# Kernel optimization log

Hardware: AMD Instinct MI355X
Metric: run time of the kernel (lower is better)

Reference implementation:

```python
import jax, jax.numpy as jnp
import numpy as np

HID = 32
R = 3
B = 2
IN = 64
N = 100000
E = 1600000
G = 256


def setup_inputs() -> dict:
    key = jax.random.key(0)
    ks = jax.random.split(key, 16)
    x = jax.random.normal(ks[0], (N, IN), dtype=jnp.float32)
    src = jax.random.randint(ks[1], (E,), 0, N)
    dst = jax.random.randint(ks[2], (E,), 0, N)
    etype = jax.random.randint(ks[3], (E,), 0, R)
    graph_ids = jnp.sort(jax.random.randint(ks[4], (N,), 0, G))
    s = 0.05
    basis1 = jax.random.normal(ks[5], (B, IN, HID), dtype=jnp.float32) * s   # layer 1 basis
    basis_r = jax.random.normal(ks[6], (3, B, HID, HID), dtype=jnp.float32) * s  # layers 2-4
    w_comp = jax.random.normal(ks[7], (4, R, B), dtype=jnp.float32) * s     # per-layer basis coeffs
    loop1 = jax.random.normal(ks[8], (IN, HID), dtype=jnp.float32) * s
    loop_r = jax.random.normal(ks[9], (3, HID, HID), dtype=jnp.float32) * s
    bias = jnp.zeros((4, HID), dtype=jnp.float32)
    lin1_w = jax.random.normal(ks[10], (4 * HID, 64), dtype=jnp.float32) * s
    lin1_b = jnp.zeros((64,), dtype=jnp.float32)
    lin2_w = jax.random.normal(ks[11], (64, 1), dtype=jnp.float32) * s
    lin2_b = jnp.zeros((1,), dtype=jnp.float32)
    return dict(x=x, basis1=basis1, basis_r=basis_r, w_comp=w_comp, loop1=loop1,
                loop_r=loop_r, bias=bias, lin1_w=lin1_w, lin1_b=lin1_b,
                lin2_w=lin2_w, lin2_b=lin2_b, src=src, dst=dst, etype=etype,
                graph_ids=graph_ids, num_graphs=G)


def _rel_conv(h, basis, comp, loop_w, b, src, dst, etype, n_nodes):
    # basis-decomposed relation weights: W[r] = sum_b comp[r,b] * basis[b]
    W = jnp.einsum('rb,bio->rio', comp, basis)            # [R, in, out]
    h_rel = jnp.einsum('ni,rio->rno', h, W)               # [R, N, out]
    msg = h_rel[etype, src]                               # [E, out] edge-typed gather
    agg = jax.ops.segment_sum(msg, dst, num_segments=n_nodes)
    return agg + h @ loop_w + b                           # self-loop + bias


def reference(x, basis1, basis_r, w_comp, loop1, loop_r, bias,
              lin1_w, lin1_b, lin2_w, lin2_b,
              src, dst, etype, graph_ids, num_graphs):
    n = x.shape[0]
    h = jnp.tanh(_rel_conv(x, basis1, w_comp[0], loop1, bias[0], src, dst, etype, n))
    states = [h]
    for i in range(3):
        h = jnp.tanh(_rel_conv(h, basis_r[i], w_comp[i + 1], loop_r[i], bias[i + 1],
                               src, dst, etype, n))
        states.append(h)
    feat = jnp.concatenate(states, axis=1)                # [N, 128]
    # mean-pool nodes per graph (diff_pooling ~ dgl mean_nodes)
    summed = jax.ops.segment_sum(feat, graph_ids, num_segments=num_graphs)
    counts = jax.ops.segment_sum(jnp.ones((n,), feat.dtype), graph_ids,
                                 num_segments=num_graphs)
    pooled = summed / jnp.maximum(counts, 1.0)[:, None]   # [G, 128]
    hdn = jax.nn.relu(pooled @ lin1_w + lin1_b)
    out = jax.nn.sigmoid(hdn @ lin2_w + lin2_b)
    return out[:, 0]
```

## Files before the change

### kernel.cpp

```cpp
#include <hip/hip_runtime.h>
#include <cstdint>
#include <cmath>

#define DLO_BITS 7
#define DLO_MASK 127

__global__ __launch_bounds__(256) void prep_w1(
    const float* __restrict__ basis1,
    const float* __restrict__ w_comp,
    float* __restrict__ W1)
{
    int tid = blockIdx.x * 256 + threadIdx.x;
    if (tid < 6144) {
        int r = tid / 2048, io = tid % 2048;
        W1[tid] = w_comp[r*2] * basis1[io] + w_comp[r*2+1] * basis1[2048 + io];
    }
}

__global__ __launch_bounds__(256) void count_kernel(
    const int* __restrict__ dst, int* __restrict__ bcnt, int E, int NB)
{
    __shared__ int cnt[1024];
    for (int i = threadIdx.x; i < NB; i += 256) cnt[i] = 0;
    __syncthreads();
    int base = blockIdx.x * 4096;
    #pragma unroll
    for (int i = 0; i < 16; ++i) {
        int e = base + i * 256 + threadIdx.x;
        if (e < E) atomicAdd(&cnt[dst[e] >> DLO_BITS], 1);
    }
    __syncthreads();
    for (int i = threadIdx.x; i < NB; i += 256)
        if (cnt[i]) atomicAdd(&bcnt[i], cnt[i]);
}

__global__ __launch_bounds__(1024) void scan_kernel(
    const int* __restrict__ bcnt, int* __restrict__ bbase,
    int* __restrict__ bcur, int NB)
{
    __shared__ int s[1024];
    int t = threadIdx.x;
    int v = (t < NB) ? bcnt[t] : 0;
    s[t] = v; __syncthreads();
    for (int off = 1; off < 1024; off <<= 1) {
        int u = (t >= off) ? s[t - off] : 0;
        __syncthreads();
        s[t] += u;
        __syncthreads();
    }
    if (t < NB) { int b = s[t] - v; bbase[t] = b; bcur[t] = b; }
}

__global__ __launch_bounds__(256) void bscatter_kernel(
    const int* __restrict__ src, const int* __restrict__ dst,
    const int* __restrict__ et, int* __restrict__ bcur,
    unsigned* __restrict__ eidx1, int E, int NB)
{
    __shared__ int cnt[1024];
    __shared__ int bbs[1024];
    int tid = threadIdx.x;
    for (int i = tid; i < NB; i += 256) cnt[i] = 0;
    __syncthreads();
    int base = blockIdx.x * 8192;
    int lim = E - base; if (lim > 8192) lim = 8192;
    for (int i = tid; i < lim; i += 256)
        atomicAdd(&cnt[dst[base + i] >> DLO_BITS], 1);
    __syncthreads();
    for (int i = tid; i < NB; i += 256) {
        int c = cnt[i];
        bbs[i] = c ? atomicAdd(&bcur[i], c) : 0;
    }
    __syncthreads();
    for (int i = tid; i < NB; i += 256) cnt[i] = 0;
    __syncthreads();
    for (int i = tid; i < lim; i += 256) {
        int e = base + i;
        int d = dst[e];
        int bk = d >> DLO_BITS;
        int p = bbs[bk] + atomicAdd(&cnt[bk], 1);
        eidx1[p] = (unsigned)src[e] | ((unsigned)et[e] << 17)
                 | ((unsigned)(d & DLO_MASK) << 19);
    }
}

__global__ __launch_bounds__(256) void bucket_sort_kernel(
    const unsigned* __restrict__ eidx1, const int* __restrict__ bbase,
    const int* __restrict__ bcnt, unsigned* __restrict__ eidx2,
    int* __restrict__ row_ptr, int* __restrict__ deg, int N)
{
    __shared__ int c128[128], excl[128], w[128];
    int tid = threadIdx.x, b = blockIdx.x;
    int gbase = bbase[b], cnt = bcnt[b], n0 = b << DLO_BITS;
    if (tid < 128) c128[tid] = 0;
    __syncthreads();
    for (int k = tid; k < cnt; k += 256)
        atomicAdd(&c128[(eidx1[gbase + k] >> 19) & DLO_MASK], 1);
    __syncthreads();
    if (tid < 128) w[tid] = c128[tid];
    __syncthreads();
    for (int off = 1; off < 128; off <<= 1) {
        int u = (tid < 128 && tid >= off) ? w[tid - off] : 0;
        __syncthreads();
        if (tid < 128) w[tid] += u;
        __syncthreads();
    }
    if (tid < 128) {
        excl[tid] = w[tid] - c128[tid];
        int n = n0 + tid;
        if (n < N) { row_ptr[n] = gbase + excl[tid]; deg[n] = c128[tid]; }
        c128[tid] = 0;
    }
    __syncthreads();
    for (int k = tid; k < cnt; k += 256) {
        unsigned pk = eidx1[gbase + k];
        int dlo = (pk >> 19) & DLO_MASK;
        int p = excl[dlo] + atomicAdd(&c128[dlo], 1);
        eidx2[gbase + p] = pk;
    }
}

__global__ __launch_bounds__(256) void dense_kernel(
    const float* __restrict__ x,
    const float* __restrict__ Wrel,
    const float* __restrict__ Wloop,
    const float* __restrict__ bias_l,
    float* __restrict__ hrel,
    float* __restrict__ agg,
    int N)
{
    __shared__ float sW[4 * 2048];
    __shared__ float sH[64 * 68];
    const int tid = threadIdx.x;
    for (int i = tid; i < 3 * 2048; i += 256) sW[i] = Wrel[i];
    for (int i = tid; i < 2048; i += 256) sW[6144 + i] = Wloop[i];
    const int nb = blockIdx.x * 64;
    for (int idx = tid; idx < 64 * 64; idx += 256) {
        int n = idx >> 6, i = idx & 63;
        int gn = nb + n;
        sH[n * 68 + i] = (gn < N) ? x[(size_t)gn * 64 + i] : 0.0f;
    }
    __syncthreads();

    const int m  = tid >> 6;
    const int l  = tid & 63;
    const int ow = l & 7;
    const int ng = l >> 3;

    float acc[8][4];
    #pragma unroll
    for (int j = 0; j < 8; ++j)
        #pragma unroll
        for (int k = 0; k < 4; ++k) acc[j][k] = 0.0f;

    const float* wb = &sW[m * 2048 + ow * 4];
    #pragma unroll 2
    for (int i = 0; i < 64; i += 4) {
        float4 wv0 = *(const float4*)(wb + (i + 0) * 32);
        float4 wv1 = *(const float4*)(wb + (i + 1) * 32);
        float4 wv2 = *(const float4*)(wb + (i + 2) * 32);
        float4 wv3 = *(const float4*)(wb + (i + 3) * 32);
        #pragma unroll
        for (int j = 0; j < 8; ++j) {
            float4 hv = *(const float4*)&sH[(j * 8 + ng) * 68 + i];
            acc[j][0] += hv.x * wv0.x + hv.y * wv1.x + hv.z * wv2.x + hv.w * wv3.x;
            acc[j][1] += hv.x * wv0.y + hv.y * wv1.y + hv.z * wv2.y + hv.w * wv3.y;
            acc[j][2] += hv.x * wv0.z + hv.y * wv1.z + hv.z * wv2.z + hv.w * wv3.z;
            acc[j][3] += hv.x * wv0.w + hv.y * wv1.w + hv.z * wv2.w + hv.w * wv3.w;
        }
    }

    if (m < 3) {
        #pragma unroll
        for (int j = 0; j < 8; ++j) {
            int n = nb + j * 8 + ng;
            if (n < N)
                *(float4*)&hrel[((size_t)m * N + n) * 32 + ow * 4] =
                    make_float4(acc[j][0], acc[j][1], acc[j][2], acc[j][3]);
        }
    } else {
        float4 bb = *(const float4*)&bias_l[ow * 4];
        #pragma unroll
        for (int j = 0; j < 8; ++j) {
            int n = nb + j * 8 + ng;
            if (n < N)
                *(float4*)&agg[(size_t)n * 32 + ow * 4] =
                    make_float4(acc[j][0] + bb.x, acc[j][1] + bb.y,
                                acc[j][2] + bb.z, acc[j][3] + bb.w);
        }
    }
}

__global__ __launch_bounds__(256) void gather1_kernel(
    const unsigned* __restrict__ eidx, const int* __restrict__ row_ptr,
    const int* __restrict__ deg, const float* __restrict__ hrel,
    const float* __restrict__ agg, float* __restrict__ feat, int N)
{
    int tid = blockIdx.x * 256 + threadIdx.x;
    int n = tid >> 3;
    if (n >= N) return;
    int c = (tid & 7) << 2;
    int base = row_ptr[n], cnt = deg[n];
    const float4 bv = *(const float4*)&agg[(size_t)n * 32 + c];
    float a0[4] = {bv.x, bv.y, bv.z, bv.w};
    float a1[4] = {0, 0, 0, 0}, a2[4] = {0, 0, 0, 0}, a3[4] = {0, 0, 0, 0};
    int k = 0;
    for (; k + 4 <= cnt; k += 4) {
        unsigned p0 = eidx[base + k + 0], p1 = eidx[base + k + 1];
        unsigned p2 = eidx[base + k + 2], p3 = eidx[base + k + 3];
        float4 v0 = *(const float4*)&hrel[(((size_t)((p0 >> 17) & 3)) * N + (p0 & 0x1FFFF)) * 32 + c];
        float4 v1 = *(const float4*)&hrel[(((size_t)((p1 >> 17) & 3)) * N + (p1 & 0x1FFFF)) * 32 + c];
        float4 v2 = *(const float4*)&hrel[(((size_t)((p2 >> 17) & 3)) * N + (p2 & 0x1FFFF)) * 32 + c];
        float4 v3 = *(const float4*)&hrel[(((size_t)((p3 >> 17) & 3)) * N + (p3 & 0x1FFFF)) * 32 + c];
        a0[0] += v0.x; a0[1] += v0.y; a0[2] += v0.z; a0[3] += v0.w;
        a1[0] += v1.x; a1[1] += v1.y; a1[2] += v1.z; a1[3] += v1.w;
        a2[0] += v2.x; a2[1] += v2.y; a2[2] += v2.z; a2[3] += v2.w;
        a3[0] += v3.x; a3[1] += v3.y; a3[2] += v3.z; a3[3] += v3.w;
    }
    for (; k < cnt; ++k) {
        unsigned p = eidx[base + k];
        float4 v = *(const float4*)&hrel[(((size_t)((p >> 17) & 3)) * N + (p & 0x1FFFF)) * 32 + c];
        a0[0] += v.x; a0[1] += v.y; a0[2] += v.z; a0[3] += v.w;
    }
    float r0 = a0[0] + a1[0] + a2[0] + a3[0];
    float r1 = a0[1] + a1[1] + a2[1] + a3[1];
    float r2 = a0[2] + a1[2] + a2[2] + a3[2];
    float r3 = a0[3] + a1[3] + a2[3] + a3[3];
    float4* out = (float4*)&feat[(size_t)n * 128 + c];
    *out = make_float4(tanhf(r0), tanhf(r1), tanhf(r2), tanhf(r3));
}

__global__ __launch_bounds__(256) void fused_layer_kernel(
    const unsigned* __restrict__ eidx, const int* __restrict__ row_ptr,
    const int* __restrict__ deg,
    const float* __restrict__ basis_b,
    const float* __restrict__ loop_w,
    const float* __restrict__ bias_l,
    const float* __restrict__ comp,
    const float* __restrict__ feat_in,
    float* __restrict__ feat_out,
    int N)
{
    __shared__ float sB0[1024], sB1[1024], sL[1024];
    __shared__ float sT0[32 * 36], sT1[32 * 36], sH[32 * 36];
    const int tid = threadIdx.x;
    for (int i = tid; i < 1024; i += 256) {
        sB0[i] = basis_b[i];
        sB1[i] = basis_b[1024 + i];
        sL[i]  = loop_w[i];
    }
    const float cc0r0 = comp[0], cc1r0 = comp[1];
    const float cc0r1 = comp[2], cc1r1 = comp[3];
    const float cc0r2 = comp[4], cc1r2 = comp[5];

    const int nn = tid >> 3, cg = (tid & 7) << 2;
    const int n = blockIdx.x * 32 + nn;

    float4 h4 = *(const float4*)&feat_in[(size_t)n * 128 + cg];
    *(float4*)&sH[nn * 36 + cg] = h4;

    const int base = row_ptr[n], cnt = deg[n];
    float t0a[4] = {0,0,0,0}, t1a[4] = {0,0,0,0};
    float t0b[4] = {0,0,0,0}, t1b[4] = {0,0,0,0};
    int k = 0;
    for (; k + 4 <= cnt; k += 4) {
        unsigned p0 = eidx[base + k + 0], p1 = eidx[base + k + 1];
        unsigned p2 = eidx[base + k + 2], p3 = eidx[base + k + 3];
        int r0 = (p0 >> 17) & 3, r1 = (p1 >> 17) & 3;
        int r2 = (p2 >> 17) & 3, r3 = (p3 >> 17) & 3;
        float4 v0 = *(const float4*)&feat_in[(size_t)(p0 & 0x1FFFF) * 128 + cg];
        float4 v1 = *(const float4*)&feat_in[(size_t)(p1 & 0x1FFFF) * 128 + cg];
        float4 v2 = *(const float4*)&feat_in[(size_t)(p2 & 0x1FFFF) * 128 + cg];
        float4 v3 = *(const float4*)&feat_in[(size_t)(p3 & 0x1FFFF) * 128 + cg];
        float c00 = r0 == 0 ? cc0r0 : (r0 == 1 ? cc0r1 : cc0r2);
        float c10 = r0 == 0 ? cc1r0 : (r0 == 1 ? cc1r1 : cc1r2);
        float c01 = r1 == 0 ? cc0r0 : (r1 == 1 ? cc0r1 : cc0r2);
        float c11 = r1 == 0 ? cc1r0 : (r1 == 1 ? cc1r1 : cc1r2);
        float c02 = r2 == 0 ? cc0r0 : (r2 == 1 ? cc0r1 : cc0r2);
        float c12 = r2 == 0 ? cc1r0 : (r2 == 1 ? cc1r1 : cc1r2);
        float c03 = r3 == 0 ? cc0r0 : (r3 == 1 ? cc0r1 : cc0r2);
        float c13 = r3 == 0 ? cc1r0 : (r3 == 1 ? cc1r1 : cc1r2);
        t0a[0] += c00*v0.x; t0a[1] += c00*v0.y; t0a[2] += c00*v0.z; t0a[3] += c00*v0.w;
        t1a[0] += c10*v0.x; t1a[1] += c10*v0.y; t1a[2] += c10*v0.z; t1a[3] += c10*v0.w;
        t0b[0] += c01*v1.x; t0b[1] += c01*v1.y; t0b[2] += c01*v1.z; t0b[3] += c01*v1.w;
        t1b[0] += c11*v1.x; t1b[1] += c11*v1.y; t1b[2] += c11*v1.z; t1b[3] += c11*v1.w;
        t0a[0] += c02*v2.x; t0a[1] += c02*v2.y; t0a[2] += c02*v2.z; t0a[3] += c02*v2.w;
        t1a[0] += c12*v2.x; t1a[1] += c12*v2.y; t1a[2] += c12*v2.z; t1a[3] += c12*v2.w;
        t0b[0] += c03*v3.x; t0b[1] += c03*v3.y; t0b[2] += c03*v3.z; t0b[3] += c03*v3.w;
        t1b[0] += c13*v3.x; t1b[1] += c13*v3.y; t1b[2] += c13*v3.z; t1b[3] += c13*v3.w;
    }
    for (; k < cnt; ++k) {
        unsigned p = eidx[base + k];
        int r = (p >> 17) & 3;
        float4 v = *(const float4*)&feat_in[(size_t)(p & 0x1FFFF) * 128 + cg];
        float c0 = r == 0 ? cc0r0 : (r == 1 ? cc0r1 : cc0r2);
        float c1 = r == 0 ? cc1r0 : (r == 1 ? cc1r1 : cc1r2);
        t0a[0] += c0*v.x; t0a[1] += c0*v.y; t0a[2] += c0*v.z; t0a[3] += c0*v.w;
        t1a[0] += c1*v.x; t1a[1] += c1*v.y; t1a[2] += c1*v.z; t1a[3] += c1*v.w;
    }
    *(float4*)&sT0[nn * 36 + cg] = make_float4(t0a[0]+t0b[0], t0a[1]+t0b[1],
                                               t0a[2]+t0b[2], t0a[3]+t0b[3]);
    *(float4*)&sT1[nn * 36 + cg] = make_float4(t1a[0]+t1b[0], t1a[1]+t1b[1],
                                               t1a[2]+t1b[2], t1a[3]+t1b[3]);
    __syncthreads();

    float4 bb = *(const float4*)&bias_l[cg];
    float a[4] = {bb.x, bb.y, bb.z, bb.w};
    #pragma unroll 8
    for (int kk = 0; kk < 32; ++kk) {
        float p0 = sT0[nn * 36 + kk];
        float p1 = sT1[nn * 36 + kk];
        float hh = sH[nn * 36 + kk];
        float4 b0 = *(const float4*)&sB0[kk * 32 + cg];
        float4 b1 = *(const float4*)&sB1[kk * 32 + cg];
        float4 lw = *(const float4*)&sL[kk * 32 + cg];
        a[0] += p0 * b0.x + p1 * b1.x + hh * lw.x;
        a[1] += p0 * b0.y + p1 * b1.y + hh * lw.y;
        a[2] += p0 * b0.z + p1 * b1.z + hh * lw.z;
        a[3] += p0 * b0.w + p1 * b1.w + hh * lw.w;
    }
    *(float4*)&feat_out[(size_t)n * 128 + cg] =
        make_float4(tanhf(a[0]), tanhf(a[1]), tanhf(a[2]), tanhf(a[3]));
}

__global__ __launch_bounds__(256) void pool_kernel(
    const float* __restrict__ feat, const int* __restrict__ gid,
    float* __restrict__ pooled, float* __restrict__ cntArr, int N)
{
    int chunk0 = blockIdx.x * 128;
    int ch = threadIdx.x & 127, half = threadIdx.x >> 7;
    int n = chunk0 + half;
    int lim = chunk0 + 128; if (lim > N) lim = N;
    if (n >= lim) return;
    int cur = gid[n];
    float acc = 0.0f; int cc = 0;
    for (; n < lim; n += 2) {
        int g = gid[n];
        if (g != cur) {
            atomicAdd(&pooled[(size_t)cur * 128 + ch], acc);
            if (ch == 0) atomicAdd(&cntArr[cur], (float)cc);
            acc = 0.0f; cc = 0; cur = g;
        }
        acc += feat[(size_t)n * 128 + ch];
        ++cc;
    }
    atomicAdd(&pooled[(size_t)cur * 128 + ch], acc);
    if (ch == 0) atomicAdd(&cntArr[cur], (float)cc);
}

__global__ __launch_bounds__(64) void mlp_kernel(
    const float* __restrict__ pooled, const float* __restrict__ cntArr,
    const float* __restrict__ w1, const float* __restrict__ b1,
    const float* __restrict__ w2, const float* __restrict__ b2,
    float* __restrict__ out)
{
    int g = blockIdx.x;
    int t = threadIdx.x;
    float inv = 1.0f / fmaxf(cntArr[g], 1.0f);
    float acc = b1[t];
    #pragma unroll 8
    for (int k = 0; k < 128; ++k)
        acc += pooled[(size_t)g * 128 + k] * inv * w1[k * 64 + t];
    float h = fmaxf(acc, 0.0f);
    float p = h * w2[t];
    #pragma unroll
    for (int off = 32; off > 0; off >>= 1) p += __shfl_down(p, off, 64);
    if (t == 0) out[g] = 1.0f / (1.0f + expf(-(p + b2[0])));
}

extern "C" void kernel_launch(void* const* d_in, const int* in_sizes, int n_in,
                              void* d_out, int out_size, void* d_ws, size_t ws_size,
                              hipStream_t stream)
{
    const float* x       = (const float*)d_in[0];
    const float* basis1  = (const float*)d_in[1];
    const float* basis_r = (const float*)d_in[2];
    const float* w_comp  = (const float*)d_in[3];
    const float* loop1   = (const float*)d_in[4];
    const float* loop_r  = (const float*)d_in[5];
    const float* bias    = (const float*)d_in[6];
    const float* lin1_w  = (const float*)d_in[7];
    const float* lin1_b  = (const float*)d_in[8];
    const float* lin2_w  = (const float*)d_in[9];
    const float* lin2_b  = (const float*)d_in[10];
    const int*   src     = (const int*)d_in[11];
    const int*   dst     = (const int*)d_in[12];
    const int*   etype   = (const int*)d_in[13];
    const int*   gid     = (const int*)d_in[14];

    const int N = in_sizes[0] / 64;
    const int E = in_sizes[11];
    const int G = out_size;
    const int NB = (N + DLO_MASK) >> DLO_BITS;

    float* ws      = (float*)d_ws;
    float* W1      = ws;
    float* hrel    = W1 + 6144;
    float* agg     = hrel + (size_t)3 * N * 32;
    float* feat    = agg + (size_t)N * 32;
    float* pooled  = feat + (size_t)N * 128;
    float* cntArr  = pooled + (size_t)G * 128;
    int*   bcnt    = (int*)(cntArr + G);
    int*   bbase   = bcnt + NB;
    int*   bcur    = bbase + NB;
    int*   row_ptr = bcur + NB;
    int*   deg     = row_ptr + N;
    unsigned* eidx2 = (unsigned*)(deg + N);
    unsigned* eidx1 = (unsigned*)feat;

    hipMemsetAsync(pooled, 0, ((size_t)G * 128 + G + NB) * sizeof(float), stream);
    prep_w1<<<24, 256, 0, stream>>>(basis1, w_comp, W1);

    count_kernel<<<(E + 4095) / 4096, 256, 0, stream>>>(dst, bcnt, E, NB);
    scan_kernel<<<1, 1024, 0, stream>>>(bcnt, bbase, bcur, NB);
    bscatter_kernel<<<(E + 8191) / 8192, 256, 0, stream>>>(src, dst, etype, bcur, eidx1, E, NB);
    bucket_sort_kernel<<<NB, 256, 0, stream>>>(eidx1, bbase, bcnt, eidx2, row_ptr, deg, N);

    dense_kernel<<<(N + 63) / 64, 256, 0, stream>>>(x, W1, loop1, bias, hrel, agg, N);
    gather1_kernel<<<(N * 8 + 255) / 256, 256, 0, stream>>>(eidx2, row_ptr, deg, hrel, agg, feat, N);

    for (int l = 1; l < 4; ++l) {
        fused_layer_kernel<<<(N + 31) / 32, 256, 0, stream>>>(
            eidx2, row_ptr, deg,
            basis_r + (size_t)(l - 1) * 2048,
            loop_r + (size_t)(l - 1) * 1024,
            bias + l * 32,
            w_comp + l * 6,
            feat + (l - 1) * 32,
            feat + l * 32,
            N);
    }

    pool_kernel<<<NB, 256, 0, stream>>>(feat, gid, pooled, cntArr, N);
    mlp_kernel<<<G, 64, 0, stream>>>(pooled, cntArr, lin1_w, lin1_b, lin2_w, lin2_b, (float*)d_out);
}
```

Measured before the change: 313.6 us.

## Fold W1 prep into dense kernel, read x directly, shrink scatter chunks

New measurement: 375.6 us. 19.8% more time.

```diff
diff --git a/kernel.cpp b/kernel.cpp
--- a/kernel.cpp
+++ b/kernel.cpp
@@ -4,18 +4,7 @@
 
 #define DLO_BITS 7
 #define DLO_MASK 127
-
-__global__ __launch_bounds__(256) void prep_w1(
-    const float* __restrict__ basis1,
-    const float* __restrict__ w_comp,
-    float* __restrict__ W1)
-{
-    int tid = blockIdx.x * 256 + threadIdx.x;
-    if (tid < 6144) {
-        int r = tid / 2048, io = tid % 2048;
-        W1[tid] = w_comp[r*2] * basis1[io] + w_comp[r*2+1] * basis1[2048 + io];
-    }
-}
+#define SCAT_Q 2048
 
 __global__ __launch_bounds__(256) void count_kernel(
     const int* __restrict__ dst, int* __restrict__ bcnt, int E, int NB)
@@ -23,9 +12,9 @@
     __shared__ int cnt[1024];
     for (int i = threadIdx.x; i < NB; i += 256) cnt[i] = 0;
     __syncthreads();
-    int base = blockIdx.x * 4096;
+    int base = blockIdx.x * SCAT_Q;
     #pragma unroll
-    for (int i = 0; i < 16; ++i) {
+    for (int i = 0; i < SCAT_Q / 256; ++i) {
         int e = base + i * 256 + threadIdx.x;
         if (e < E) atomicAdd(&cnt[dst[e] >> DLO_BITS], 1);
     }
@@ -61,8 +50,8 @@
     int tid = threadIdx.x;
     for (int i = tid; i < NB; i += 256) cnt[i] = 0;
     __syncthreads();
-    int base = blockIdx.x * 8192;
-    int lim = E - base; if (lim > 8192) lim = 8192;
+    int base = blockIdx.x * SCAT_Q;
+    int lim = E - base; if (lim > SCAT_Q) lim = SCAT_Q;
     for (int i = tid; i < lim; i += 256)
         atomicAdd(&cnt[dst[base + i] >> DLO_BITS], 1);
     __syncthreads();
@@ -86,7 +75,7 @@
 __global__ __launch_bounds__(256) void bucket_sort_kernel(
     const unsigned* __restrict__ eidx1, const int* __restrict__ bbase,
     const int* __restrict__ bcnt, unsigned* __restrict__ eidx2,
-    int* __restrict__ row_ptr, int* __restrict__ deg, int N)
+    int* __restrict__ rp, int* __restrict__ rend, int N)
 {
     __shared__ int c128[128], excl[128], w[128];
     int tid = threadIdx.x, b = blockIdx.x;
@@ -107,7 +96,7 @@
     if (tid < 128) {
         excl[tid] = w[tid] - c128[tid];
         int n = n0 + tid;
-        if (n < N) { row_ptr[n] = gbase + excl[tid]; deg[n] = c128[tid]; }
+        if (n < N) { rp[n] = gbase + excl[tid]; rend[n] = gbase + excl[tid] + c128[tid]; }
         c128[tid] = 0;
     }
     __syncthreads();
@@ -119,25 +108,24 @@
     }
 }
 
-__global__ __launch_bounds__(256) void dense_kernel(
+__global__ __launch_bounds__(256, 4) void dense_kernel(
     const float* __restrict__ x,
-    const float* __restrict__ Wrel,
-    const float* __restrict__ Wloop,
+    const float* __restrict__ basis1,
+    const float* __restrict__ loop1,
+    const float* __restrict__ w_comp,
     const float* __restrict__ bias_l,
     float* __restrict__ hrel,
     float* __restrict__ agg,
     int N)
 {
     __shared__ float sW[4 * 2048];
-    __shared__ float sH[64 * 68];
     const int tid = threadIdx.x;
-    for (int i = tid; i < 3 * 2048; i += 256) sW[i] = Wrel[i];
-    for (int i = tid; i < 2048; i += 256) sW[6144 + i] = Wloop[i];
-    const int nb = blockIdx.x * 64;
-    for (int idx = tid; idx < 64 * 64; idx += 256) {
-        int n = idx >> 6, i = idx & 63;
-        int gn = nb + n;
-        sH[n * 68 + i] = (gn < N) ? x[(size_t)gn * 64 + i] : 0.0f;
+    for (int i = tid; i < 4 * 2048; i += 256) {
+        int m = i >> 11, io = i & 2047;
+        float v;
+        if (m < 3) v = w_comp[m * 2] * basis1[io] + w_comp[m * 2 + 1] * basis1[2048 + io];
+        else       v = loop1[io];
+        sW[i] = v;
     }
     __syncthreads();
 
@@ -145,6 +133,15 @@
     const int l  = tid & 63;
     const int ow = l & 7;
     const int ng = l >> 3;
+    const int nb = blockIdx.x * 64;
+
+    const float* xr[8];
+    #pragma unroll
+    for (int j = 0; j < 8; ++j) {
+        int gn = nb + j * 8 + ng;
+        if (gn > N - 1) gn = N - 1;
+        xr[j] = x + (size_t)gn * 64;
+    }
 
     float acc[8][4];
     #pragma unroll
@@ -161,7 +158,7 @@
         float4 wv3 = *(const float4*)(wb + (i + 3) * 32);
         #pragma unroll
         for (int j = 0; j < 8; ++j) {
-            float4 hv = *(const float4*)&sH[(j * 8 + ng) * 68 + i];
+            float4 hv = *(const float4*)(xr[j] + i);
             acc[j][0] += hv.x * wv0.x + hv.y * wv1.x + hv.z * wv2.x + hv.w * wv3.x;
             acc[j][1] += hv.x * wv0.y + hv.y * wv1.y + hv.z * wv2.y + hv.w * wv3.y;
             acc[j][2] += hv.x * wv0.z + hv.y * wv1.z + hv.z * wv2.z + hv.w * wv3.z;
@@ -191,15 +188,15 @@
 }
 
 __global__ __launch_bounds__(256) void gather1_kernel(
-    const unsigned* __restrict__ eidx, const int* __restrict__ row_ptr,
-    const int* __restrict__ deg, const float* __restrict__ hrel,
+    const unsigned* __restrict__ eidx, const int* __restrict__ rp,
+    const int* __restrict__ rend, const float* __restrict__ hrel,
     const float* __restrict__ agg, float* __restrict__ feat, int N)
 {
     int tid = blockIdx.x * 256 + threadIdx.x;
     int n = tid >> 3;
     if (n >= N) return;
     int c = (tid & 7) << 2;
-    int base = row_ptr[n], cnt = deg[n];
+    int base = rp[n], cnt = rend[n] - base;
     const float4 bv = *(const float4*)&agg[(size_t)n * 32 + c];
     float a0[4] = {bv.x, bv.y, bv.z, bv.w};
     float a1[4] = {0, 0, 0, 0}, a2[4] = {0, 0, 0, 0}, a3[4] = {0, 0, 0, 0};
@@ -230,8 +227,8 @@
 }
 
 __global__ __launch_bounds__(256) void fused_layer_kernel(
-    const unsigned* __restrict__ eidx, const int* __restrict__ row_ptr,
-    const int* __restrict__ deg,
+    const unsigned* __restrict__ eidx, const int* __restrict__ rp,
+    const int* __restrict__ rend,
     const float* __restrict__ basis_b,
     const float* __restrict__ loop_w,
     const float* __restrict__ bias_l,
@@ -258,7 +255,7 @@
     float4 h4 = *(const float4*)&feat_in[(size_t)n * 128 + cg];
     *(float4*)&sH[nn * 36 + cg] = h4;
 
-    const int base = row_ptr[n], cnt = deg[n];
+    const int base = rp[n], cnt = rend[n] - base;
     float t0a[4] = {0,0,0,0}, t1a[4] = {0,0,0,0};
     float t0b[4] = {0,0,0,0}, t1b[4] = {0,0,0,0};
     int k = 0;
@@ -393,8 +390,7 @@
     const int NB = (N + DLO_MASK) >> DLO_BITS;
 
     float* ws      = (float*)d_ws;
-    float* W1      = ws;
-    float* hrel    = W1 + 6144;
+    float* hrel    = ws;
     float* agg     = hrel + (size_t)3 * N * 32;
     float* feat    = agg + (size_t)N * 32;
     float* pooled  = feat + (size_t)N * 128;
@@ -402,25 +398,25 @@
     int*   bcnt    = (int*)(cntArr + G);
     int*   bbase   = bcnt + NB;
     int*   bcur    = bbase + NB;
-    int*   row_ptr = bcur + NB;
-    int*   deg     = row_ptr + N;
-    unsigned* eidx2 = (unsigned*)(deg + N);
+    int*   rp      = bcur + NB;
+    int*   rend    = rp + N;
+    unsigned* eidx2 = (unsigned*)(rend + N);
     unsigned* eidx1 = (unsigned*)feat;
 
     hipMemsetAsync(pooled, 0, ((size_t)G * 128 + G + NB) * sizeof(float), stream);
-    prep_w1<<<24, 256, 0, stream>>>(basis1, w_comp, W1);
-
-    count_kernel<<<(E + 4095) / 4096, 256, 0, stream>>>(dst, bcnt, E, NB);
+
+    const int nsb = (E + SCAT_Q - 1) / SCAT_Q;
+    count_kernel<<<nsb, 256, 0, stream>>>(dst, bcnt, E, NB);
     scan_kernel<<<1, 1024, 0, stream>>>(bcnt, bbase, bcur, NB);
-    bscatter_kernel<<<(E + 8191) / 8192, 256, 0, stream>>>(src, dst, etype, bcur, eidx1, E, NB);
-    bucket_sort_kernel<<<NB, 256, 0, stream>>>(eidx1, bbase, bcnt, eidx2, row_ptr, deg, N);
-
-    dense_kernel<<<(N + 63) / 64, 256, 0, stream>>>(x, W1, loop1, bias, hrel, agg, N);
-    gather1_kernel<<<(N * 8 + 255) / 256, 256, 0, stream>>>(eidx2, row_ptr, deg, hrel, agg, feat, N);
+    bscatter_kernel<<<nsb, 256, 0, stream>>>(src, dst, etype, bcur, eidx1, E, NB);
+    bucket_sort_kernel<<<NB, 256, 0, stream>>>(eidx1, bbase, bcnt, eidx2, rp, rend, N);
+
+    dense_kernel<<<(N + 63) / 64, 256, 0, stream>>>(x, basis1, loop1, w_comp, bias, hrel, agg, N);
+    gather1_kernel<<<(N * 8 + 255) / 256, 256, 0, stream>>>(eidx2, rp, rend, hrel, agg, feat, N);
 
     for (int l = 1; l < 4; ++l) {
         fused_layer_kernel<<<(N + 31) / 32, 256, 0, stream>>>(
-            eidx2, row_ptr, deg,
+            eidx2, rp, rend,
             basis_r + (size_t)(l - 1) * 2048,
             loop_r + (size_t)(l - 1) * 1024,
             bias + l * 32,
@@ -430,6 +426,6 @@
             N);
     }
 
-    pool_kernel<<<NB, 256, 0, stream>>>(feat, gid, pooled, cntArr, N);
+    pool_kernel<<<(N + 127) / 128, 256, 0, stream>>>(feat, gid, pooled, cntArr, N);
     mlp_kernel<<<G, 64, 0, stream>>>(pooled, cntArr, lin1_w, lin1_b, lin2_w, lin2_b, (float*)d_out);
 }
```
